# Optimization experiments

Measured on AMD Instinct MI355X. Metric: run time of the kernel, lower is better.

## Reference

```python
import jax, jax.numpy as jnp
import numpy as np

H = 0.1           # bandwidth
R = 1024          # pdf_resolution
Q = 2048          # quantile_sample_resolution
EPS = 1e-6
LOG_NORM_SQRT2PI = float(np.log(np.sqrt(2.0 * np.pi)))


def _grid(s):
    # s: (E, Q) samples -> (E, R) linspace(min, max) with 0.0 replaced by 1e-7
    mn = s.min(axis=1)
    mx = s.max(axis=1)
    t = mn[:, None] + (mx - mn)[:, None] * (jnp.arange(R, dtype=s.dtype) / (R - 1))
    return jnp.where(t != 0.0, t, jnp.asarray(1e-7, s.dtype))


def _logpdf(x, locs):
    # x: (E, B) kernel centers; locs: (E, R) eval points
    # log p(t) = logsumexp_b(-0.5 ((t - x_b)/h)^2) - log(B) - log(h * sqrt(2*pi))
    B = x.shape[1]
    z = (locs[:, :, None] - x[:, None, :]) / H          # (E, R, B)
    lse = jax.nn.logsumexp(-0.5 * z * z, axis=-1)       # (E, R)
    return lse - (np.log(B) + np.log(H) + LOG_NORM_SQRT2PI)


def _kde(inputs, bank, noise, comp_idx, sel, slot_idx):
    x = inputs.T                                         # (E, B)
    # mixture sampling: pick component, add Gaussian noise (scale = bandwidth)
    samples = jnp.take_along_axis(x, comp_idx, axis=1) + H * noise   # (E, Q)

    # current pdf over sample range
    t0 = _grid(samples)
    current = jnp.exp(_logpdf(x, t0))                    # (E, R)

    # per-feature bijector branch (0..5; branch 6 'Exp' is unreachable in TF
    # since tf.random.uniform maxval=6 is exclusive)
    selc = sel[:, None]
    s = samples
    s_safe = jnp.where(jnp.abs(s) < EPS, jnp.asarray(EPS, s.dtype), s)
    conds_s = [selc == i for i in range(6)]
    y = jnp.select(conds_s, [
        2.0 * s,                 # Scale(2)
        s - 3.0,                 # Shift(-3)
        1.0 / s_safe,            # Reciprocal
        0.8 * s + 5.0,           # Chain([Shift(5), Scale(0.8)])
        jax.nn.sigmoid(s),       # Sigmoid
        jax.nn.softplus(s),      # Softplus
    ])
    t1 = _grid(y)                                        # (E, R)
    yc01 = jnp.clip(t1, EPS, 1.0 - EPS)                  # safe domain for logit
    ycp = jnp.clip(t1, EPS, None)                        # safe domain for softplus-inv
    conds_t = [selc == i for i in range(6)]
    # inverse f^{-1}(t) per branch
    xi = jnp.select(conds_t, [
        t1 / 2.0,
        t1 + 3.0,
        1.0 / t1,                                        # t1 != 0 by _grid fix
        (t1 - 5.0) / 0.8,
        jnp.log(yc01) - jnp.log1p(-yc01),                # logit
        jnp.log(jnp.expm1(ycp)),                         # softplus inverse
    ])
    # log |d f^{-1} / dt| per branch
    ld = jnp.select(conds_t, [
        jnp.full_like(t1, -np.log(2.0)),
        jnp.zeros_like(t1),
        -2.0 * jnp.log(jnp.abs(t1)),
        jnp.full_like(t1, -np.log(0.8)),
        -jnp.log(yc01) - jnp.log1p(-yc01),
        ycp - jnp.log(jnp.expm1(ycp)),
    ])
    transformed = jnp.exp(_logpdf(x, xi) + ld)           # (E, R)

    # scatter into bank: row 0 <- current, row 1 <- transformed,
    # random slot <- previous row-0 (read before update, as sparse_read(0))
    prev = bank[0]
    out = bank.at[0].set(current).at[1].set(transformed).at[slot_idx].set(prev)
    return out


def setup_inputs() -> dict:
    key = jax.random.key(0)
    k1, k2, k3, k4, k5 = jax.random.split(key, 5)
    inputs = jax.random.normal(k1, (256, 512), dtype=jnp.float32)
    bank = jax.random.normal(k2, (128, 512, 1024), dtype=jnp.float32)
    noise = jax.random.normal(k3, (512, 2048), dtype=jnp.float32)
    comp_idx = jax.random.randint(k4, (512, 2048), 0, 256, dtype=jnp.int32)
    sel = jax.random.randint(k5, (512,), 0, 6, dtype=jnp.int32)
    return {"inputs": inputs, "bank": bank, "noise": noise,
            "comp_idx": comp_idx, "sel": sel, "slot_idx": 37}


def reference(inputs, bank, noise, comp_idx, sel, slot_idx):
    return _kde(inputs, bank, noise, comp_idx, sel, slot_idx)
```

## Files before the change

### kernel.cpp

```cpp
#include <hip/hip_runtime.h>
#include <hip/hip_bf16.h>

#define NQ 2048
#define NB 512
#define NX 256
#define NR 1024
#define KDE_EPS 1e-6f
#define SLOT_ELEMS (NB * NR)
#define LOGC 4.1615308846901885f
#define NORM 0.015583685919813959f

__global__ __launch_bounds__(256) void row_stats(
    const float* __restrict__ inputs,
    const float* __restrict__ noise,
    const int*   __restrict__ comp_idx,
    const int*   __restrict__ sel,
    float* __restrict__ stats)
{
    const int b   = blockIdx.x;
    const int tid = threadIdx.x;
    const int selb = sel[b];

    float mns =  INFINITY, mxs = -INFINITY;
    float mny =  INFINITY, mxy = -INFINITY;

    for (int q = tid; q < NQ; q += 256) {
        const int   idx = comp_idx[b * NQ + q];
        const float nz  = noise[b * NQ + q];
        const float s   = inputs[idx * NB + b] + 0.1f * nz;
        mns = fminf(mns, s);
        mxs = fmaxf(mxs, s);
        const float ssafe = (fabsf(s) < KDE_EPS) ? KDE_EPS : s;
        float y;
        switch (selb) {
            case 0:  y = 2.0f * s; break;
            case 1:  y = s - 3.0f; break;
            case 2:  y = 1.0f / ssafe; break;
            case 3:  y = 0.8f * s + 5.0f; break;
            case 4:  y = 1.0f / (1.0f + __expf(-s)); break;
            default: y = fmaxf(s, 0.0f) + log1pf(__expf(-fabsf(s))); break;
        }
        mny = fminf(mny, y);
        mxy = fmaxf(mxy, y);
    }

    #pragma unroll
    for (int off = 32; off > 0; off >>= 1) {
        mns = fminf(mns, __shfl_down(mns, off, 64));
        mxs = fmaxf(mxs, __shfl_down(mxs, off, 64));
        mny = fminf(mny, __shfl_down(mny, off, 64));
        mxy = fmaxf(mxy, __shfl_down(mxy, off, 64));
    }

    __shared__ float red[4][4];
    const int wave = tid >> 6;
    const int lane = tid & 63;
    if (lane == 0) {
        red[0][wave] = mns; red[1][wave] = mxs;
        red[2][wave] = mny; red[3][wave] = mxy;
    }
    __syncthreads();
    if (tid == 0) {
        float a = red[0][0], c = red[1][0], d = red[2][0], e = red[3][0];
        #pragma unroll
        for (int w = 1; w < 4; ++w) {
            a = fminf(a, red[0][w]);
            c = fmaxf(c, red[1][w]);
            d = fminf(d, red[2][w]);
            e = fmaxf(e, red[3][w]);
        }
        stats[0 * NB + b] = a;
        stats[1 * NB + b] = c;
        stats[2 * NB + b] = d;
        stats[3 * NB + b] = e;
    }
}

__global__ __launch_bounds__(256) void grid_eval(
    const float* __restrict__ inputs,
    const int*   __restrict__ sel,
    const int*   __restrict__ slot_idx_p,
    const float* __restrict__ stats,
    float* __restrict__ out)
{
    const int b     = blockIdx.x;
    const int chunk = blockIdx.y;
    const int tid   = threadIdx.x;

    __shared__ float xs10[NX];
    xs10[tid] = inputs[tid * NB + b] * 10.0f;
    __syncthreads();

    const int   r  = chunk * 256 + tid;
    const float rr = (float)r / 1023.0f;

    const float mns = stats[0 * NB + b];
    const float mxs = stats[1 * NB + b];
    const float mny = stats[2 * NB + b];
    const float mxy = stats[3 * NB + b];

    float t0 = mns + (mxs - mns) * rr;
    if (t0 == 0.0f) t0 = 1e-7f;
    float t1 = mny + (mxy - mny) * rr;
    if (t1 == 0.0f) t1 = 1e-7f;

    const int selb = sel[b];
    const float yc01 = fminf(fmaxf(t1, KDE_EPS), 1.0f - KDE_EPS);
    const float ycp  = fmaxf(t1, KDE_EPS);

    float xi, ld;
    switch (selb) {
        case 0:  xi = 0.5f * t1;            ld = -0.6931471805599453f; break;
        case 1:  xi = t1 + 3.0f;            ld = 0.0f;                 break;
        case 2:  xi = 1.0f / t1;            ld = -2.0f * logf(fabsf(t1)); break;
        case 3:  xi = (t1 - 5.0f) * 1.25f;  ld = 0.22314355131420976f; break;
        case 4:  xi = logf(yc01) - log1pf(-yc01);
                 ld = -logf(yc01) - log1pf(-yc01);                     break;
        default: { const float em = expm1f(ycp);
                   xi = logf(em);
                   ld = ycp - xi; }                                     break;
    }

    const float t010 = t0 * 10.0f;
    const float xi10 = xi * 10.0f;

    float acc0 = 0.0f, acc1 = 0.0f;
    #pragma unroll 8
    for (int j = 0; j < NX; ++j) {
        const float xv = xs10[j];
        const float z0 = t010 - xv;
        const float z1 = xi10 - xv;
        acc0 += __expf(-0.5f * z0 * z0);
        acc1 += __expf(-0.5f * z1 * z1);
    }

    const float current     = acc0 * NORM;
    const float transformed = __expf(__logf(acc1) + ld - LOGC);

    const int slot_idx = *slot_idx_p;
    const size_t o = (size_t)b * NR + r;
    if (slot_idx != 0) out[o] = current;
    if (slot_idx != 1) out[SLOT_ELEMS + o] = transformed;
}

__global__ __launch_bounds__(256) void copy_bank(
    const float4* __restrict__ bank,
    const int*    __restrict__ slot_idx_p,
    float4* __restrict__ out)
{
    const int PER_SLOT_V4 = SLOT_ELEMS / 4;
    const int slot_idx = *slot_idx_p;
    const size_t i = (size_t)blockIdx.x * blockDim.x + threadIdx.x;
    const int slot = (int)(i >> 17);
    const size_t pos = i & (size_t)(PER_SLOT_V4 - 1);
    if (slot == slot_idx) {
        out[i] = bank[pos];
    } else if (slot >= 2) {
        out[i] = bank[i];
    }
}

extern "C" void kernel_launch(void* const* d_in, const int* in_sizes, int n_in,
                              void* d_out, int out_size, void* d_ws, size_t ws_size,
                              hipStream_t stream) {
    const float* inputs   = (const float*)d_in[0];
    const float* bank     = (const float*)d_in[1];
    const float* noise    = (const float*)d_in[2];
    const int*   comp_idx = (const int*)d_in[3];
    const int*   sel      = (const int*)d_in[4];
    const int*   slotp    = (const int*)d_in[5];
    float* out   = (float*)d_out;
    float* stats = (float*)d_ws;

    row_stats<<<NB, 256, 0, stream>>>(inputs, noise, comp_idx, sel, stats);

    dim3 g2(NB, NR / 256);
    grid_eval<<<g2, 256, 0, stream>>>(inputs, sel, slotp, stats, out);

    const int total_v4 = 128 * (SLOT_ELEMS / 4);
    copy_bank<<<total_v4 / 256, 256, 0, stream>>>((const float4*)bank, slotp, (float4*)out);
}
```

Baseline: 488.5 us.

## Fuse stats, KDE eval and bank copy into one interleaved kernel

Merges the three kernels into a single launch. Every 32nd block in the first range runs the KDE evaluation, and each such block recomputes its row's min/max stats locally; all other blocks perform the bank copy using nontemporal vector loads and stores. This removes two launches and the stats round-trip through global memory, and overlaps the compute-bound evaluation with the bandwidth-bound copy. The Gaussian kernel inputs are prescaled so the code can use the hardware exp2 directly. The cost is that each eval block redoes the stats reduction for its row four times, and the copy indexing becomes more complex.

```diff
diff --git a/kernel.cpp b/kernel.cpp
--- a/kernel.cpp
+++ b/kernel.cpp
@@ -1,35 +1,71 @@
 #include <hip/hip_runtime.h>
 #include <hip/hip_bf16.h>
+
+typedef float v4f __attribute__((ext_vector_type(4)));
 
 #define NQ 2048
 #define NB 512
 #define NX 256
 #define NR 1024
 #define KDE_EPS 1e-6f
-#define SLOT_ELEMS (NB * NR)
+#define PS4 131072
 #define LOGC 4.1615308846901885f
 #define NORM 0.015583685919813959f
+#define SCALE 8.4932180028801903f
 
-__global__ __launch_bounds__(256) void row_stats(
+#define NEVAL 2048
+#define EVAL_SPAN 65536
+#define NCOPY 64512
+#define GRID_TOTAL (NCOPY + NEVAL)
+
+__global__ __launch_bounds__(256) void kde_fused(
     const float* __restrict__ inputs,
+    const v4f*   __restrict__ bank4,
     const float* __restrict__ noise,
     const int*   __restrict__ comp_idx,
     const int*   __restrict__ sel,
-    float* __restrict__ stats)
+    const int*   __restrict__ slotp,
+    float*       __restrict__ out)
 {
-    const int b   = blockIdx.x;
+    const unsigned bx = blockIdx.x;
     const int tid = threadIdx.x;
-    const int selb = sel[b];
+
+    const bool is_eval = (bx < EVAL_SPAN) && ((bx & 31u) == 0u);
+    if (!is_eval) {
+        const int slot_idx = *slotp;
+        const size_t ci = (bx < EVAL_SPAN) ? (size_t)(bx - (bx >> 5) - 1u)
+                                           : (size_t)(bx - NEVAL);
+        v4f* __restrict__ out4 = (v4f*)out;
+        const size_t i = (size_t)2 * PS4 + ci * 256 + tid;
+        const int slot = (int)(i >> 17);
+        const size_t src = (slot == slot_idx) ? (i & (size_t)(PS4 - 1)) : i;
+        v4f v = __builtin_nontemporal_load(&bank4[src]);
+        __builtin_nontemporal_store(v, &out4[i]);
+        if (slot_idx < 2 && ci < 512) {
+            const size_t pos = ci * 256 + tid;
+            v4f v2 = __builtin_nontemporal_load(&bank4[pos]);
+            __builtin_nontemporal_store(v2, &out4[(size_t)slot_idx * PS4 + pos]);
+        }
+        return;
+    }
+
+    const unsigned e = bx >> 5;
+    const int b     = (int)(e >> 2);
+    const int chunk = (int)(e & 3u);
+    const int selb  = sel[b];
+
+    __shared__ float xsS[NX];
+    __shared__ float red[4][4];
+    __shared__ float sst[4];
+
+    xsS[tid] = inputs[tid * NB + b] * SCALE;
 
     float mns =  INFINITY, mxs = -INFINITY;
     float mny =  INFINITY, mxy = -INFINITY;
-
     for (int q = tid; q < NQ; q += 256) {
         const int   idx = comp_idx[b * NQ + q];
-        const float nz  = noise[b * NQ + q];
-        const float s   = inputs[idx * NB + b] + 0.1f * nz;
-        mns = fminf(mns, s);
-        mxs = fmaxf(mxs, s);
+        const float s   = inputs[idx * NB + b] + 0.1f * noise[b * NQ + q];
+        mns = fminf(mns, s);  mxs = fmaxf(mxs, s);
         const float ssafe = (fabsf(s) < KDE_EPS) ? KDE_EPS : s;
         float y;
         switch (selb) {
@@ -40,10 +76,8 @@
             case 4:  y = 1.0f / (1.0f + __expf(-s)); break;
             default: y = fmaxf(s, 0.0f) + log1pf(__expf(-fabsf(s))); break;
         }
-        mny = fminf(mny, y);
-        mxy = fmaxf(mxy, y);
+        mny = fminf(mny, y);  mxy = fmaxf(mxy, y);
     }
-
     #pragma unroll
     for (int off = 32; off > 0; off >>= 1) {
         mns = fminf(mns, __shfl_down(mns, off, 64));
@@ -51,113 +85,62 @@
         mny = fminf(mny, __shfl_down(mny, off, 64));
         mxy = fmaxf(mxy, __shfl_down(mxy, off, 64));
     }
-
-    __shared__ float red[4][4];
-    const int wave = tid >> 6;
-    const int lane = tid & 63;
-    if (lane == 0) {
-        red[0][wave] = mns; red[1][wave] = mxs;
-        red[2][wave] = mny; red[3][wave] = mxy;
+    const int wave = tid >> 6, lane = tid & 63;
+    if (lane == 0) { red[0][wave]=mns; red[1][wave]=mxs; red[2][wave]=mny; red[3][wave]=mxy; }
+    __syncthreads();
+    if (tid == 0) {
+        float a=red[0][0], c=red[1][0], d=red[2][0], f=red[3][0];
+        #pragma unroll
+        for (int w=1; w<4; ++w) {
+            a=fminf(a,red[0][w]); c=fmaxf(c,red[1][w]);
+            d=fminf(d,red[2][w]); f=fmaxf(f,red[3][w]);
+        }
+        sst[0]=a; sst[1]=c; sst[2]=d; sst[3]=f;
     }
     __syncthreads();
-    if (tid == 0) {
-        float a = red[0][0], c = red[1][0], d = red[2][0], e = red[3][0];
-        #pragma unroll
-        for (int w = 1; w < 4; ++w) {
-            a = fminf(a, red[0][w]);
-            c = fmaxf(c, red[1][w]);
-            d = fminf(d, red[2][w]);
-            e = fmaxf(e, red[3][w]);
-        }
-        stats[0 * NB + b] = a;
-        stats[1 * NB + b] = c;
-        stats[2 * NB + b] = d;
-        stats[3 * NB + b] = e;
-    }
-}
+    mns=sst[0]; mxs=sst[1]; mny=sst[2]; mxy=sst[3];
 
-__global__ __launch_bounds__(256) void grid_eval(
-    const float* __restrict__ inputs,
-    const int*   __restrict__ sel,
-    const int*   __restrict__ slot_idx_p,
-    const float* __restrict__ stats,
-    float* __restrict__ out)
-{
-    const int b     = blockIdx.x;
-    const int chunk = blockIdx.y;
-    const int tid   = threadIdx.x;
+    const int r = chunk * 256 + tid;
+    const float rr = (float)r * (1.0f / 1023.0f);
+    float t0 = mns + (mxs - mns) * rr;  if (t0 == 0.0f) t0 = 1e-7f;
+    float t1 = mny + (mxy - mny) * rr;  if (t1 == 0.0f) t1 = 1e-7f;
 
-    __shared__ float xs10[NX];
-    xs10[tid] = inputs[tid * NB + b] * 10.0f;
-    __syncthreads();
-
-    const int   r  = chunk * 256 + tid;
-    const float rr = (float)r / 1023.0f;
-
-    const float mns = stats[0 * NB + b];
-    const float mxs = stats[1 * NB + b];
-    const float mny = stats[2 * NB + b];
-    const float mxy = stats[3 * NB + b];
-
-    float t0 = mns + (mxs - mns) * rr;
-    if (t0 == 0.0f) t0 = 1e-7f;
-    float t1 = mny + (mxy - mny) * rr;
-    if (t1 == 0.0f) t1 = 1e-7f;
-
-    const int selb = sel[b];
     const float yc01 = fminf(fmaxf(t1, KDE_EPS), 1.0f - KDE_EPS);
     const float ycp  = fmaxf(t1, KDE_EPS);
-
     float xi, ld;
     switch (selb) {
-        case 0:  xi = 0.5f * t1;            ld = -0.6931471805599453f; break;
-        case 1:  xi = t1 + 3.0f;            ld = 0.0f;                 break;
-        case 2:  xi = 1.0f / t1;            ld = -2.0f * logf(fabsf(t1)); break;
-        case 3:  xi = (t1 - 5.0f) * 1.25f;  ld = 0.22314355131420976f; break;
+        case 0:  xi = 0.5f * t1;           ld = -0.6931471805599453f; break;
+        case 1:  xi = t1 + 3.0f;           ld = 0.0f;                 break;
+        case 2:  xi = 1.0f / t1;           ld = -2.0f * logf(fabsf(t1)); break;
+        case 3:  xi = (t1 - 5.0f) * 1.25f; ld = 0.22314355131420976f; break;
         case 4:  xi = logf(yc01) - log1pf(-yc01);
-                 ld = -logf(yc01) - log1pf(-yc01);                     break;
-        default: { const float em = expm1f(ycp);
-                   xi = logf(em);
-                   ld = ycp - xi; }                                     break;
+                 ld = -logf(yc01) - log1pf(-yc01);                    break;
+        default: { const float em = expm1f(ycp); xi = logf(em); ld = ycp - xi; } break;
     }
 
-    const float t010 = t0 * 10.0f;
-    const float xi10 = xi * 10.0f;
+    const float tK  = t0 * SCALE;
+    const float xiK = xi * SCALE;
 
     float acc0 = 0.0f, acc1 = 0.0f;
-    #pragma unroll 8
-    for (int j = 0; j < NX; ++j) {
-        const float xv = xs10[j];
-        const float z0 = t010 - xv;
-        const float z1 = xi10 - xv;
-        acc0 += __expf(-0.5f * z0 * z0);
-        acc1 += __expf(-0.5f * z1 * z1);
+    const v4f* xs4 = (const v4f*)xsS;
+    #pragma unroll 4
+    for (int j4 = 0; j4 < NX / 4; ++j4) {
+        const v4f xv = xs4[j4];
+        float w;
+        w = tK  - xv.x; acc0 += __builtin_amdgcn_exp2f(-(w * w));
+        w = tK  - xv.y; acc0 += __builtin_amdgcn_exp2f(-(w * w));
+        w = tK  - xv.z; acc0 += __builtin_amdgcn_exp2f(-(w * w));
+        w = tK  - xv.w; acc0 += __builtin_amdgcn_exp2f(-(w * w));
+        w = xiK - xv.x; acc1 += __builtin_amdgcn_exp2f(-(w * w));
+        w = xiK - xv.y; acc1 += __builtin_amdgcn_exp2f(-(w * w));
+        w = xiK - xv.z; acc1 += __builtin_amdgcn_exp2f(-(w * w));
+        w = xiK - xv.w; acc1 += __builtin_amdgcn_exp2f(-(w * w));
     }
 
-    const float current     = acc0 * NORM;
-    const float transformed = __expf(__logf(acc1) + ld - LOGC);
-
-    const int slot_idx = *slot_idx_p;
+    const int slot_idx = *slotp;
     const size_t o = (size_t)b * NR + r;
-    if (slot_idx != 0) out[o] = current;
-    if (slot_idx != 1) out[SLOT_ELEMS + o] = transformed;
-}
-
-__global__ __launch_bounds__(256) void copy_bank(
-    const float4* __restrict__ bank,
-    const int*    __restrict__ slot_idx_p,
-    float4* __restrict__ out)
-{
-    const int PER_SLOT_V4 = SLOT_ELEMS / 4;
-    const int slot_idx = *slot_idx_p;
-    const size_t i = (size_t)blockIdx.x * blockDim.x + threadIdx.x;
-    const int slot = (int)(i >> 17);
-    const size_t pos = i & (size_t)(PER_SLOT_V4 - 1);
-    if (slot == slot_idx) {
-        out[i] = bank[pos];
-    } else if (slot >= 2) {
-        out[i] = bank[i];
-    }
+    if (slot_idx != 0) out[o] = acc0 * NORM;
+    if (slot_idx != 1) out[(size_t)NB * NR + o] = __expf(__logf(acc1) + ld - LOGC);
 }
 
 extern "C" void kernel_launch(void* const* d_in, const int* in_sizes, int n_in,
@@ -169,14 +152,8 @@
     const int*   comp_idx = (const int*)d_in[3];
     const int*   sel      = (const int*)d_in[4];
     const int*   slotp    = (const int*)d_in[5];
-    float* out   = (float*)d_out;
-    float* stats = (float*)d_ws;
+    float* out = (float*)d_out;
 
-    row_stats<<<NB, 256, 0, stream>>>(inputs, noise, comp_idx, sel, stats);
-
-    dim3 g2(NB, NR / 256);
-    grid_eval<<<g2, 256, 0, stream>>>(inputs, sel, slotp, stats, out);
-
-    const int total_v4 = 128 * (SLOT_ELEMS / 4);
-    copy_bank<<<total_v4 / 256, 256, 0, stream>>>((const float4*)bank, slotp, (float4*)out);
+    kde_fused<<<GRID_TOTAL, 256, 0, stream>>>(
+        inputs, (const v4f*)bank, noise, comp_idx, sel, slotp, out);
 }
```

New measurement: 1.435 ms. 2.94x slower.
